# Kernel tuning notes

Measured on AMD Instinct MI355X. Metric: run time of the kernel, lower is better.

The kernel has to match this reference:

```python
import jax, jax.numpy as jnp
import numpy as np

BATCH, N, C_IN, HID, C_OUT = 32, 4096, 128, 256, 128


def setup_inputs() -> dict:
    key = jax.random.key(0)
    k1, k2, k3, k4 = jax.random.split(key, 4)
    x = jax.random.normal(k1, (BATCH, N, C_IN), dtype=jnp.float32)
    A = jnp.eye(HID, dtype=jnp.float32) + 0.01 * jax.random.normal(k2, (HID, HID), dtype=jnp.float32)
    W_B = 0.01 * jax.random.normal(k3, (HID, C_IN), dtype=jnp.float32)
    W_C = 0.01 * jax.random.normal(k4, (C_OUT, HID), dtype=jnp.float32)
    return {"x": x, "A": A, "W_B": W_B, "W_C": W_C}


def reference(x, A, W_B, W_C):
    # Spectral-norm normalize A (torch.linalg.norm ord=2 = largest singular value)
    A_norm = A / (jnp.linalg.norm(A, ord=2) + 1e-5)
    # Precompute input projection for all timesteps: (B, N, H)
    u = jnp.einsum('bnc,hc->bnh', x, W_B)

    h0 = jnp.zeros((x.shape[0], A.shape[0]), dtype=x.dtype)

    def step(h, u_t):
        h = jax.nn.relu(h @ A_norm.T + u_t)
        return h, h

    # scan over time axis: (N, B, H)
    _, hs = jax.lax.scan(step, h0, jnp.swapaxes(u, 0, 1))
    # Output projection applied to all hidden states at once: (B, N, C_out)
    y = jnp.einsum('nbh,oh->bno', hs, W_C)
    return y
```

## Files before the change

### kernel.cpp

```cpp
#include <hip/hip_runtime.h>
#include <hip/hip_bf16.h>
#include <hip/hip_fp16.h>

#define DEV static __device__ __forceinline__

typedef unsigned int u32;
typedef unsigned short u16;

typedef _Float16 half2v __attribute__((ext_vector_type(2)));

union HU { u32 u; half2v h; };
union FI { float f; int i; };

#if __has_builtin(__builtin_amdgcn_fdot2)
DEV float fdot2u(u32 a, u32 b, float c){
  HU ua; ua.u = a; HU ub; ub.u = b;
  return __builtin_amdgcn_fdot2(ua.h, ub.h, c, false);
}
#else
DEV float fdot2u(u32 a, u32 b, float c){
  HU ua; ua.u = a; HU ub; ub.u = b;
  return c + (float)ua.h.x*(float)ub.h.x + (float)ua.h.y*(float)ub.h.y;
}
#endif

#if __has_builtin(__builtin_amdgcn_mov_dpp)
DEV float dppf(float x, const int ctrl_b1, const int ctrl_4e, const int sel){
  FI u; u.f = x;
  if (sel == 0)      u.i = __builtin_amdgcn_mov_dpp(u.i, 0xB1, 0xF, 0xF, true);
  else if (sel == 1) u.i = __builtin_amdgcn_mov_dpp(u.i, 0x4E, 0xF, 0xF, true);
  else               u.i = __builtin_amdgcn_mov_dpp(u.i, 0x128, 0xF, 0xF, true);
  return u.f;
  (void)ctrl_b1; (void)ctrl_4e;
}
#define XOR1F(x) dppf((x),0,0,0)
#define XOR2F(x) dppf((x),0,0,1)
#define XOR8F(x) dppf((x),0,0,2)
#else
#define XOR1F(x) __shfl_xor((x), 1, 64)
#define XOR2F(x) __shfl_xor((x), 2, 64)
#define XOR8F(x) __shfl_xor((x), 8, 64)
#endif

#if __has_builtin(__builtin_amdgcn_ds_swizzle)
DEV float xor4f(float x){
  FI u; u.f = x;
  u.i = __builtin_amdgcn_ds_swizzle(u.i, 0x101F);
  return u.f;
}
#else
DEV float xor4f(float x){ return __shfl_xor(x, 4, 64); }
#endif

DEV u32 packh2(float x, float y){
  half2v h; h.x = (_Float16)x; h.y = (_Float16)y;
  HU u; u.h = h; return u.u;
}

DEV float bf2f(u16 v){ u32 x = ((u32)v) << 16; float f; __builtin_memcpy(&f, &x, 4); return f; }

DEV u16 f2bf(float f){
  u32 x; __builtin_memcpy(&x, &f, 4);
  u32 r = (x + 0x7fffu + ((x >> 16) & 1u)) >> 16;
  return (u16)r;
}

DEV float4 load4g(const void* p, long g, int bf){
  if (!bf) return ((const float4*)p)[g];
  ushort4 u = ((const ushort4*)p)[g];
  return make_float4(bf2f(u.x), bf2f(u.y), bf2f(u.z), bf2f(u.w));
}
DEV float load1g(const void* p, long i, int bf){
  return bf ? bf2f(((const u16*)p)[i]) : ((const float*)p)[i];
}

DEV int mloc(int v){ return (v & 3) | ((v & 8) >> 1); }

__global__ void k_detect(const void* __restrict__ A, int* __restrict__ flag){
  float a0 = ((const float*)A)[0];
  *flag = !(a0 > 0.5f && a0 < 2.0f);
}

__global__ __launch_bounds__(256) void k_btb(const void* __restrict__ A, float* __restrict__ Bm,
                                             const int* __restrict__ flag){
  __shared__ float acol[256];
  int t = threadIdx.x, r = blockIdx.x, bf = *flag;
  acol[t] = load1g(A, (long)t*256 + r, bf);
  __syncthreads();
  float acc = 0.f;
  if (bf){
    const u16* Ab = (const u16*)A;
    #pragma unroll 4
    for (int k = 0; k < 256; k++) acc += acol[k] * bf2f(Ab[(long)k*256 + t]);
  } else {
    const float* Af = (const float*)A;
    #pragma unroll 4
    for (int k = 0; k < 256; k++) acc += acol[k] * Af[(long)k*256 + t];
  }
  Bm[(long)r*256 + t] = acc;
}

__global__ __launch_bounds__(512) void k_lanczos(const float* __restrict__ Bm, float* __restrict__ out_scale){
  const int NIT = 40;
  __shared__ float vbuf[256], vprev[256];
  __shared__ float part[2][256];
  __shared__ float red[8];
  __shared__ float al[NIT], be[NIT + 1];
  int tid = threadIdx.x;
  int i = tid & 255, kh = tid >> 8;

  float4 Breg[32];
  #pragma unroll
  for (int g = 0; g < 32; g++) Breg[g] = ((const float4*)Bm)[(long)i*64 + kh*32 + g];

  if (tid == 0) be[0] = 0.f;
  if (tid < 256){
    u32 rs = (u32)tid*1103515245u + 12345u;
    rs ^= rs >> 13; rs *= 2654435761u; rs ^= rs >> 16;
    vbuf[tid] = (float)(rs & 0xffffu)/32768.0f - 1.0f;
    vprev[tid] = 0.f;
  }
  __syncthreads();
  if (tid < 256){
    float p = vbuf[tid]*vbuf[tid];
    #pragma unroll
    for (int m = 1; m < 64; m <<= 1) p += __shfl_xor(p, m, 64);
    if ((tid & 63) == 0) red[tid >> 6] = p;
  }
  __syncthreads();
  {
    float nv = rsqrtf(red[0]+red[1]+red[2]+red[3]);
    if (tid < 256) vbuf[tid] *= nv;
  }
  __syncthreads();

  float bprev = 0.f;
  for (int it = 0; it < NIT; it++){
    const float4* vb4 = (const float4*)vbuf;
    float4 acc = {0.f,0.f,0.f,0.f};
    #pragma unroll
    for (int g = 0; g < 32; g++){
      float4 bq = Breg[g]; float4 v = vb4[kh*32 + g];
      acc.x += bq.x*v.x; acc.y += bq.y*v.y; acc.z += bq.z*v.z; acc.w += bq.w*v.w;
    }
    part[kh][i] = acc.x+acc.y+acc.z+acc.w;
    __syncthreads();
    float w = 0.f;
    if (tid < 256){
      w = part[0][tid] + part[1][tid];
      float p = w * vbuf[tid];
      #pragma unroll
      for (int m = 1; m < 64; m <<= 1) p += __shfl_xor(p, m, 64);
      if ((tid & 63) == 0) red[tid >> 6] = p;
    }
    __syncthreads();
    float alpha = red[0]+red[1]+red[2]+red[3];
    if (tid == 0) al[it] = alpha;
    __syncthreads();
    if (tid < 256){
      w -= alpha*vbuf[tid] + bprev*vprev[tid];
      float p = w*w;
      #pragma unroll
      for (int m = 1; m < 64; m <<= 1) p += __shfl_xor(p, m, 64);
      if ((tid & 63) == 0) red[tid >> 6] = p;
    }
    __syncthreads();
    float bnew = sqrtf(fmaxf(red[0]+red[1]+red[2]+red[3], 0.f));
    if (tid == 0) be[it+1] = bnew;
    if (tid < 256){
      vprev[tid] = vbuf[tid];
      vbuf[tid] = (bnew > 1e-12f) ? (w / bnew) : 0.f;
    }
    bprev = bnew;
    __syncthreads();
  }

  if (tid < 64){
    float amax = -1e30f, gmax = -1e30f;
    for (int q = 0; q < NIT; q++){
      float b0 = (q > 0)       ? be[q]   : 0.f;
      float b1 = (q < NIT-1)   ? be[q+1] : 0.f;
      gmax = fmaxf(gmax, al[q] + fabsf(b0) + fabsf(b1));
      amax = fmaxf(amax, al[q]);
    }
    float lo = amax - 1e-4f, hi = gmax + 1e-3f;
    for (int r = 0; r < 4; r++){
      float step = (hi - lo) * (1.0f/65.0f);
      float cand = lo + step * (float)(tid + 1);
      int cnt = 0;
      float dd = al[0] - cand;
      if (dd < 0.f) cnt++;
      for (int q = 1; q < NIT; q++){
        float bq = be[q];
        if (fabsf(dd) < 1e-25f) dd = -1e-25f;
        dd = (al[q] - cand) - bq*bq/dd;
        if (dd < 0.f) cnt++;
      }
      unsigned long long mask = __ballot(cnt >= NIT);
      if (mask == 0ull){
        lo = lo + step*64.f;
      } else {
        int bb = __ffsll((long long)mask) - 1;
        float nlo = lo + step*(float)bb;
        float nhi = lo + step*(float)(bb+1);
        lo = nlo; hi = nhi;
      }
    }
    if (tid == 0){
      float lam = fmaxf(0.5f*(lo + hi), 1e-12f);
      *out_scale = 1.0f/(sqrtf(lam) + 1e-5f);
    }
  }
}

__global__ __launch_bounds__(256) void k_uproj(const void* __restrict__ x, const void* __restrict__ WB,
                                               u32* __restrict__ scr, const int* __restrict__ flag){
  __shared__ alignas(16) u32 Wt[64*260];
  __shared__ alignas(16) u32 xt[64*36];
  int tid = threadIdx.x;
  int bf = *flag;
  long T0 = (long)blockIdx.x * 32;
  #pragma unroll
  for (int i2 = 0; i2 < 32; i2++){
    int f = tid + 256*i2;
    int cq = f & 31, h = f >> 5;
    float4 v = load4g(WB, (long)h*32 + cq, bf);
    Wt[(2*cq)*260 + h]   = packh2(v.x, v.y);
    Wt[(2*cq+1)*260 + h] = packh2(v.z, v.w);
  }
  #pragma unroll
  for (int i2 = 0; i2 < 4; i2++){
    int f = tid + 256*i2;
    int cq = f & 31, t = f >> 5;
    float4 v = load4g(x, (T0 + t)*32 + cq, bf);
    xt[(2*cq)*36 + t]   = packh2(v.x, v.y);
    xt[(2*cq+1)*36 + t] = packh2(v.z, v.w);
  }
  __syncthreads();
  int hg = tid & 63, tg = tid >> 6;
  float acc[4][8];
  #pragma unroll
  for (int a1 = 0; a1 < 4; a1++)
    for (int b1 = 0; b1 < 8; b1++) acc[a1][b1] = 0.f;
  #pragma unroll 4
  for (int kp = 0; kp < 64; kp++){
    uint4 wv = *(const uint4*)&Wt[kp*260 + 4*hg];
    uint4 xa = *(const uint4*)&xt[kp*36 + 8*tg];
    uint4 xb = *(const uint4*)&xt[kp*36 + 8*tg + 4];
    u32 wj[4] = {wv.x, wv.y, wv.z, wv.w};
    u32 xs[8] = {xa.x, xa.y, xa.z, xa.w, xb.x, xb.y, xb.z, xb.w};
    #pragma unroll
    for (int jj = 0; jj < 4; jj++)
      #pragma unroll
      for (int tt = 0; tt < 8; tt++)
        acc[jj][tt] = fdot2u(wj[jj], xs[tt], acc[jj][tt]);
  }
  #pragma unroll
  for (int tt = 0; tt < 8; tt++){
    long T = T0 + 8*tg + tt;
    uint2 o;
    o.x = packh2(acc[0][tt], acc[1][tt]);
    o.y = packh2(acc[2][tt], acc[3][tt]);
    ((uint2*)scr)[T*64 + hg] = o;
  }
}

__global__ __launch_bounds__(512, 2) void k_recur(const void* __restrict__ A, const float* __restrict__ scale_p,
                                                  u32* __restrict__ scr, const int* __restrict__ flag){
  __shared__ alignas(16) char hbuf[2][768];
  __shared__ alignas(16) __half uring[32*256];
  int tid = threadIdx.x;
  int i = tid >> 4, j = tid & 15;
  int b = blockIdx.x;
  int bf = *flag;
  float s = *scale_p;
  int myrow = 8*i + mloc(j);

  u32 a[8][8];
  #pragma unroll
  for (int sx = 0; sx < 8; sx++){
    int G = (sx & 3) | ((sx & 4) << 1);
    int R = 8*i + mloc(j ^ G);
    #pragma unroll
    for (int q = 0; q < 4; q++){
      float4 v = load4g(A, (long)R*64 + 4*j + q, bf);
      float vv[4] = {v.x, v.y, v.z, v.w};
      #pragma unroll
      for (int e = 0; e < 4; e++){
        int col = 16*j + 4*q + e;
        if (col == R) vv[e] = 0.f;
      }
      a[sx][2*q]   = packh2(vv[0]*s, vv[1]*s);
      a[sx][2*q+1] = packh2(vv[2]*s, vv[3]*s);
    }
  }
  float d = load1g(A, (long)myrow*257, bf) * s;

  const uint4* scr4 = (const uint4*)scr;
  uint4* ur4 = (uint4*)uring;
  long ubase4 = (long)b * 131072;
  u16* hsout = (u16*)scr + (long)b*4096*256;

  uint4 pf;
  ur4[tid] = scr4[ubase4 + tid];
  pf = scr4[ubase4 + 512 + tid];

  int hoff16 = 24*(myrow >> 4) + (myrow & 15);
  ((u16*)hbuf[0])[hoff16] = 0;
  ((u16*)hbuf[1])[hoff16] = 0;
  __syncthreads();

  float hprev = 0.f;
  #pragma unroll 1
  for (int t = 0; t < 4096; ++t){
    const uint4* h4 = (const uint4*)(hbuf[t & 1] + 48*j);
    uint4 h0 = h4[0], h1 = h4[1];
    float uv = __half2float(uring[(t & 31)*256 + myrow]);
    float acc[8];
    #pragma unroll
    for (int sx = 0; sx < 8; sx++){
      float ac = 0.f;
      ac = fdot2u(a[sx][0], h0.x, ac);
      ac = fdot2u(a[sx][1], h0.y, ac);
      ac = fdot2u(a[sx][2], h0.z, ac);
      ac = fdot2u(a[sx][3], h0.w, ac);
      ac = fdot2u(a[sx][4], h1.x, ac);
      ac = fdot2u(a[sx][5], h1.y, ac);
      ac = fdot2u(a[sx][6], h1.z, ac);
      ac = fdot2u(a[sx][7], h1.w, ac);
      acc[sx] = ac;
    }
    acc[0] += XOR1F(acc[1]);
    acc[2] += XOR1F(acc[3]);
    acc[4] += XOR1F(acc[5]);
    acc[6] += XOR1F(acc[7]);
    acc[0] += XOR2F(acc[2]);
    acc[4] += XOR2F(acc[6]);
    acc[0] += XOR8F(acc[4]);
    float sum = acc[0] + xor4f(acc[0]);

    float hnew = fmaxf(fmaf(d, hprev, sum + uv), 0.f);
    hprev = hnew;
    u16 hh = __half_as_ushort(__float2half(hnew));
    ((u16*)hbuf[(t & 1) ^ 1])[hoff16] = hh;
    hsout[(long)t*256 + myrow] = hh;

    if ((t & 15) == 15 && t < 4095){
      int ct = (t + 1) >> 4;
      ur4[(ct & 1)*512 + tid] = pf;
      if (ct < 255) pf = scr4[ubase4 + (long)(ct + 1)*512 + tid];
    }
    __syncthreads();
  }
}

__global__ __launch_bounds__(256) void k_yproj(const u32* __restrict__ scr, const void* __restrict__ WC,
                                               void* __restrict__ y, const int* __restrict__ flag){
  __shared__ alignas(16) u32 Wt[128*132];
  __shared__ alignas(16) u32 ht[128*68];
  int tid = threadIdx.x, bf = *flag;
  long T0 = (long)blockIdx.x * 64;
  #pragma unroll
  for (int i2 = 0; i2 < 32; i2++){
    int f = tid + 256*i2;
    int kp = f & 127, t = f >> 7;
    ht[kp*68 + t] = scr[(T0 + t)*128 + kp];
  }
  #pragma unroll
  for (int i2 = 0; i2 < 32; i2++){
    int f = tid + 256*i2;
    int kq = f & 63, o = f >> 6;
    float4 v = load4g(WC, (long)o*64 + kq, bf);
    Wt[(2*kq)*132 + o]   = packh2(v.x, v.y);
    Wt[(2*kq+1)*132 + o] = packh2(v.z, v.w);
  }
  __syncthreads();
  int og = tid & 31, tg = tid >> 5;
  float acc[4][8];
  #pragma unroll
  for (int a1 = 0; a1 < 4; a1++)
    for (int b1 = 0; b1 < 8; b1++) acc[a1][b1] = 0.f;
  #pragma unroll 4
  for (int kp = 0; kp < 128; kp++){
    uint4 wv = *(const uint4*)&Wt[kp*132 + 4*og];
    uint4 ha = *(const uint4*)&ht[kp*68 + 8*tg];
    uint4 hc = *(const uint4*)&ht[kp*68 + 8*tg + 4];
    u32 wj[4] = {wv.x, wv.y, wv.z, wv.w};
    u32 hs8[8] = {ha.x, ha.y, ha.z, ha.w, hc.x, hc.y, hc.z, hc.w};
    #pragma unroll
    for (int jj = 0; jj < 4; jj++)
      #pragma unroll
      for (int tt = 0; tt < 8; tt++)
        acc[jj][tt] = fdot2u(wj[jj], hs8[tt], acc[jj][tt]);
  }
  #pragma unroll
  for (int tt = 0; tt < 8; tt++){
    long T = T0 + 8*tg + tt;
    if (!bf){
      float4 o = {acc[0][tt], acc[1][tt], acc[2][tt], acc[3][tt]};
      ((float4*)y)[T*32 + og] = o;
    } else {
      uint2 o;
      o.x = (u32)f2bf(acc[0][tt]) | ((u32)f2bf(acc[1][tt]) << 16);
      o.y = (u32)f2bf(acc[2][tt]) | ((u32)f2bf(acc[3][tt]) << 16);
      ((uint2*)y)[T*32 + og] = o;
    }
  }
}

extern "C" void kernel_launch(void* const* d_in, const int* in_sizes, int n_in,
                              void* d_out, int out_size, void* d_ws, size_t ws_size,
                              hipStream_t stream){
  const void* x  = d_in[0];
  const void* A  = d_in[1];
  const void* WB = d_in[2];
  const void* WC = d_in[3];

  float* Bm    = (float*)d_ws;
  float* scale = (float*)((char*)d_ws + 256*1024);
  int*   flag  = (int*)((char*)d_ws + 256*1024 + 64);

  const size_t scrOff = (size_t)1 << 20;
  const size_t scrBytes = (size_t)131072 * 256 * 2;
  u32* scr = (ws_size >= scrOff + scrBytes + 4096)
               ? (u32*)((char*)d_ws + scrOff)
               : (u32*)d_out;

  k_detect <<<1, 1, 0, stream>>>(A, flag);
  k_btb    <<<256, 256, 0, stream>>>(A, Bm, flag);
  k_lanczos<<<1, 512, 0, stream>>>(Bm, scale);
  k_uproj  <<<4096, 256, 0, stream>>>(x, WB, scr, flag);
  k_recur  <<<32, 512, 0, stream>>>(A, scale, scr, flag);
  k_yproj  <<<2048, 256, 0, stream>>>(scr, WC, d_out, flag);
}
```

Before: 2.338 ms.

## Process two batch sequences per recurrence block to share barriers and weights

Each recurrence block now advances two batch sequences in lockstep instead of one, halving the grid to 16 blocks. The two independent dot-product chains give more instruction-level parallelism per barrier and spread the per-step __syncthreads and shuffle-reduction latency over twice the work, while the A fragment held in registers is reused for both sequences. The cost is more work per step on the serial critical path, higher register and LDS use, and only 16 of the GPU's CUs kept busy.

```diff
diff --git a/kernel.cpp b/kernel.cpp
--- a/kernel.cpp
+++ b/kernel.cpp
@@ -265,13 +265,38 @@
   }
 }
 
+DEV float step_dot(const u32 (&a)[8][8], uint4 h0, uint4 h1){
+  float acc[8];
+  #pragma unroll
+  for (int sx = 0; sx < 8; sx++){
+    float ac = 0.f;
+    ac = fdot2u(a[sx][0], h0.x, ac);
+    ac = fdot2u(a[sx][1], h0.y, ac);
+    ac = fdot2u(a[sx][2], h0.z, ac);
+    ac = fdot2u(a[sx][3], h0.w, ac);
+    ac = fdot2u(a[sx][4], h1.x, ac);
+    ac = fdot2u(a[sx][5], h1.y, ac);
+    ac = fdot2u(a[sx][6], h1.z, ac);
+    ac = fdot2u(a[sx][7], h1.w, ac);
+    acc[sx] = ac;
+  }
+  acc[0] += XOR1F(acc[1]);
+  acc[2] += XOR1F(acc[3]);
+  acc[4] += XOR1F(acc[5]);
+  acc[6] += XOR1F(acc[7]);
+  acc[0] += XOR2F(acc[2]);
+  acc[4] += XOR2F(acc[6]);
+  acc[0] += XOR8F(acc[4]);
+  return acc[0] + xor4f(acc[0]);
+}
+
 __global__ __launch_bounds__(512, 2) void k_recur(const void* __restrict__ A, const float* __restrict__ scale_p,
                                                   u32* __restrict__ scr, const int* __restrict__ flag){
-  __shared__ alignas(16) char hbuf[2][768];
-  __shared__ alignas(16) __half uring[32*256];
+  __shared__ alignas(16) char hbuf[2][2][768];
+  __shared__ alignas(16) __half uring[2][32*256];
   int tid = threadIdx.x;
   int i = tid >> 4, j = tid & 15;
-  int b = blockIdx.x;
+  int b0 = 2*blockIdx.x, b1 = b0 + 1;
   int bf = *flag;
   float s = *scale_p;
   int myrow = 8*i + mloc(j);
@@ -297,58 +322,57 @@
   float d = load1g(A, (long)myrow*257, bf) * s;
 
   const uint4* scr4 = (const uint4*)scr;
-  uint4* ur4 = (uint4*)uring;
-  long ubase4 = (long)b * 131072;
-  u16* hsout = (u16*)scr + (long)b*4096*256;
-
-  uint4 pf;
-  ur4[tid] = scr4[ubase4 + tid];
-  pf = scr4[ubase4 + 512 + tid];
+  uint4* ur40 = (uint4*)uring[0];
+  uint4* ur41 = (uint4*)uring[1];
+  long ub0 = (long)b0 * 131072;
+  long ub1 = (long)b1 * 131072;
+  u16* hs0 = (u16*)scr + (long)b0*4096*256;
+  u16* hs1 = (u16*)scr + (long)b1*4096*256;
+
+  uint4 pf0, pf1;
+  ur40[tid] = scr4[ub0 + tid];
+  ur41[tid] = scr4[ub1 + tid];
+  pf0 = scr4[ub0 + 512 + tid];
+  pf1 = scr4[ub1 + 512 + tid];
 
   int hoff16 = 24*(myrow >> 4) + (myrow & 15);
-  ((u16*)hbuf[0])[hoff16] = 0;
-  ((u16*)hbuf[1])[hoff16] = 0;
-  __syncthreads();
-
-  float hprev = 0.f;
+  ((u16*)hbuf[0][0])[hoff16] = 0;
+  ((u16*)hbuf[0][1])[hoff16] = 0;
+  ((u16*)hbuf[1][0])[hoff16] = 0;
+  ((u16*)hbuf[1][1])[hoff16] = 0;
+  __syncthreads();
+
+  float hp0 = 0.f, hp1 = 0.f;
   #pragma unroll 1
   for (int t = 0; t < 4096; ++t){
-    const uint4* h4 = (const uint4*)(hbuf[t & 1] + 48*j);
-    uint4 h0 = h4[0], h1 = h4[1];
-    float uv = __half2float(uring[(t & 31)*256 + myrow]);
-    float acc[8];
-    #pragma unroll
-    for (int sx = 0; sx < 8; sx++){
-      float ac = 0.f;
-      ac = fdot2u(a[sx][0], h0.x, ac);
-      ac = fdot2u(a[sx][1], h0.y, ac);
-      ac = fdot2u(a[sx][2], h0.z, ac);
-      ac = fdot2u(a[sx][3], h0.w, ac);
-      ac = fdot2u(a[sx][4], h1.x, ac);
-      ac = fdot2u(a[sx][5], h1.y, ac);
-      ac = fdot2u(a[sx][6], h1.z, ac);
-      ac = fdot2u(a[sx][7], h1.w, ac);
-      acc[sx] = ac;
-    }
-    acc[0] += XOR1F(acc[1]);
-    acc[2] += XOR1F(acc[3]);
-    acc[4] += XOR1F(acc[5]);
-    acc[6] += XOR1F(acc[7]);
-    acc[0] += XOR2F(acc[2]);
-    acc[4] += XOR2F(acc[6]);
-    acc[0] += XOR8F(acc[4]);
-    float sum = acc[0] + xor4f(acc[0]);
-
-    float hnew = fmaxf(fmaf(d, hprev, sum + uv), 0.f);
-    hprev = hnew;
-    u16 hh = __half_as_ushort(__float2half(hnew));
-    ((u16*)hbuf[(t & 1) ^ 1])[hoff16] = hh;
-    hsout[(long)t*256 + myrow] = hh;
+    const uint4* h4a = (const uint4*)(hbuf[0][t & 1] + 48*j);
+    const uint4* h4b = (const uint4*)(hbuf[1][t & 1] + 48*j);
+    uint4 ha0 = h4a[0], ha1 = h4a[1];
+    uint4 hb0 = h4b[0], hb1 = h4b[1];
+    float uv0 = __half2float(uring[0][(t & 31)*256 + myrow]);
+    float uv1 = __half2float(uring[1][(t & 31)*256 + myrow]);
+
+    float sum0 = step_dot(a, ha0, ha1);
+    float sum1 = step_dot(a, hb0, hb1);
+
+    float hn0 = fmaxf(fmaf(d, hp0, sum0 + uv0), 0.f);
+    float hn1 = fmaxf(fmaf(d, hp1, sum1 + uv1), 0.f);
+    hp0 = hn0; hp1 = hn1;
+    u16 hh0 = __half_as_ushort(__float2half(hn0));
+    u16 hh1 = __half_as_ushort(__float2half(hn1));
+    ((u16*)hbuf[0][(t & 1) ^ 1])[hoff16] = hh0;
+    ((u16*)hbuf[1][(t & 1) ^ 1])[hoff16] = hh1;
+    hs0[(long)t*256 + myrow] = hh0;
+    hs1[(long)t*256 + myrow] = hh1;
 
     if ((t & 15) == 15 && t < 4095){
       int ct = (t + 1) >> 4;
-      ur4[(ct & 1)*512 + tid] = pf;
-      if (ct < 255) pf = scr4[ubase4 + (long)(ct + 1)*512 + tid];
+      ur40[(ct & 1)*512 + tid] = pf0;
+      ur41[(ct & 1)*512 + tid] = pf1;
+      if (ct < 255){
+        pf0 = scr4[ub0 + (long)(ct + 1)*512 + tid];
+        pf1 = scr4[ub1 + (long)(ct + 1)*512 + tid];
+      }
     }
     __syncthreads();
   }
@@ -430,6 +454,6 @@
   k_btb    <<<256, 256, 0, stream>>>(A, Bm, flag);
   k_lanczos<<<1, 512, 0, stream>>>(Bm, scale);
   k_uproj  <<<4096, 256, 0, stream>>>(x, WB, scr, flag);
-  k_recur  <<<32, 512, 0, stream>>>(A, scale, scr, flag);
+  k_recur  <<<16, 512, 0, stream>>>(A, scale, scr, flag);
   k_yproj  <<<2048, 256, 0, stream>>>(scr, WC, d_out, flag);
 }
```

New measurement: 3.574 ms. +52.9%, slower.

## Use MFMA for recurrence, batching 16 sequences per block

Applied to the files above, without the earlier changes.

The recurrence kernel previously ran one block per batch element and did a matrix-vector product with packed fp16 dot instructions plus cross-lane shuffle reductions. It now runs two blocks, each handling 16 batch elements as the N dimension of a 16x16x32 fp16 MFMA. A is held in registers as MFMA A-fragments, and the hidden state sits in swizzled LDS. The u-input is prefetched through a 4-slot LDS ring. This trades parallelism across CUs (only 2 blocks) for far less arithmetic and reduction work per step, so the serial chain now depends on MFMA latency.

```diff
diff --git a/kernel.cpp b/kernel.cpp
--- a/kernel.cpp
+++ b/kernel.cpp
@@ -8,6 +8,8 @@
 typedef unsigned short u16;
 
 typedef _Float16 half2v __attribute__((ext_vector_type(2)));
+typedef _Float16 f16x8 __attribute__((ext_vector_type(8)));
+typedef float f32x4 __attribute__((ext_vector_type(4)));
 
 union HU { u32 u; half2v h; };
 union FI { float f; int i; };
@@ -24,34 +26,6 @@
 }
 #endif
 
-#if __has_builtin(__builtin_amdgcn_mov_dpp)
-DEV float dppf(float x, const int ctrl_b1, const int ctrl_4e, const int sel){
-  FI u; u.f = x;
-  if (sel == 0)      u.i = __builtin_amdgcn_mov_dpp(u.i, 0xB1, 0xF, 0xF, true);
-  else if (sel == 1) u.i = __builtin_amdgcn_mov_dpp(u.i, 0x4E, 0xF, 0xF, true);
-  else               u.i = __builtin_amdgcn_mov_dpp(u.i, 0x128, 0xF, 0xF, true);
-  return u.f;
-  (void)ctrl_b1; (void)ctrl_4e;
-}
-#define XOR1F(x) dppf((x),0,0,0)
-#define XOR2F(x) dppf((x),0,0,1)
-#define XOR8F(x) dppf((x),0,0,2)
-#else
-#define XOR1F(x) __shfl_xor((x), 1, 64)
-#define XOR2F(x) __shfl_xor((x), 2, 64)
-#define XOR8F(x) __shfl_xor((x), 8, 64)
-#endif
-
-#if __has_builtin(__builtin_amdgcn_ds_swizzle)
-DEV float xor4f(float x){
-  FI u; u.f = x;
-  u.i = __builtin_amdgcn_ds_swizzle(u.i, 0x101F);
-  return u.f;
-}
-#else
-DEV float xor4f(float x){ return __shfl_xor(x, 4, 64); }
-#endif
-
 DEV u32 packh2(float x, float y){
   half2v h; h.x = (_Float16)x; h.y = (_Float16)y;
   HU u; u.h = h; return u.u;
@@ -73,8 +47,6 @@
 DEV float load1g(const void* p, long i, int bf){
   return bf ? bf2f(((const u16*)p)[i]) : ((const float*)p)[i];
 }
-
-DEV int mloc(int v){ return (v & 3) | ((v & 8) >> 1); }
 
 __global__ void k_detect(const void* __restrict__ A, int* __restrict__ flag){
   float a0 = ((const float*)A)[0];
@@ -265,90 +237,112 @@
   }
 }
 
-__global__ __launch_bounds__(512, 2) void k_recur(const void* __restrict__ A, const float* __restrict__ scale_p,
-                                                  u32* __restrict__ scr, const int* __restrict__ flag){
-  __shared__ alignas(16) char hbuf[2][768];
-  __shared__ alignas(16) __half uring[32*256];
-  int tid = threadIdx.x;
-  int i = tid >> 4, j = tid & 15;
-  int b = blockIdx.x;
-  int bf = *flag;
-  float s = *scale_p;
-  int myrow = 8*i + mloc(j);
-
-  u32 a[8][8];
-  #pragma unroll
-  for (int sx = 0; sx < 8; sx++){
-    int G = (sx & 3) | ((sx & 4) << 1);
-    int R = 8*i + mloc(j ^ G);
-    #pragma unroll
-    for (int q = 0; q < 4; q++){
-      float4 v = load4g(A, (long)R*64 + 4*j + q, bf);
-      float vv[4] = {v.x, v.y, v.z, v.w};
-      #pragma unroll
-      for (int e = 0; e < 4; e++){
-        int col = 16*j + 4*q + e;
-        if (col == R) vv[e] = 0.f;
+__global__ __launch_bounds__(512) void k_recur(const void* __restrict__ A, const float* __restrict__ scale_p,
+                                               u32* __restrict__ scr, const int* __restrict__ flag){
+  __shared__ alignas(16) char Ht[2*8192];
+  __shared__ alignas(16) char Ur[4*8192];
+  const int tid = threadIdx.x;
+  const int w = tid >> 6, l = tid & 63;
+  const int g = l >> 4, n = l & 15;
+  const int bf = *flag;
+  const float s = *scale_p;
+  const int n0 = blockIdx.x * 16;
+
+  f16x8 af[2][8];
+  float dg[2][4];
+  #pragma unroll
+  for (int mt = 0; mt < 2; mt++){
+    int arow = 32*w + 16*mt + n;
+    #pragma unroll
+    for (int kk = 0; kk < 8; kk++){
+      int c0 = 32*kk + 8*g;
+      float4 v0 = load4g(A, (long)arow*64 + (c0 >> 2), bf);
+      float4 v1 = load4g(A, (long)arow*64 + (c0 >> 2) + 1, bf);
+      float vv[8] = {v0.x, v0.y, v0.z, v0.w, v1.x, v1.y, v1.z, v1.w};
+      f16x8 f;
+      #pragma unroll
+      for (int i2 = 0; i2 < 8; i2++){
+        float x = (c0 + i2 == arow) ? 0.f : vv[i2]*s;
+        f[i2] = (_Float16)x;
       }
-      a[sx][2*q]   = packh2(vv[0]*s, vv[1]*s);
-      a[sx][2*q+1] = packh2(vv[2]*s, vv[3]*s);
-    }
-  }
-  float d = load1g(A, (long)myrow*257, bf) * s;
-
-  const uint4* scr4 = (const uint4*)scr;
-  uint4* ur4 = (uint4*)uring;
-  long ubase4 = (long)b * 131072;
-  u16* hsout = (u16*)scr + (long)b*4096*256;
-
-  uint4 pf;
-  ur4[tid] = scr4[ubase4 + tid];
-  pf = scr4[ubase4 + 512 + tid];
-
-  int hoff16 = 24*(myrow >> 4) + (myrow & 15);
-  ((u16*)hbuf[0])[hoff16] = 0;
-  ((u16*)hbuf[1])[hoff16] = 0;
-  __syncthreads();
-
-  float hprev = 0.f;
+      af[mt][kk] = f;
+    }
+    #pragma unroll
+    for (int r = 0; r < 4; r++){
+      int R = 32*w + 16*mt + 4*g + r;
+      dg[mt][r] = load1g(A, (long)R*257, bf) * s;
+    }
+  }
+
+  const int swz = (n & 7) << 4;
+  const int R0a = 32*w + 4*g;
+
+  const uint4* u4g = (const uint4*)scr;
+  const int nb = tid >> 5, e4 = tid & 31;
+  const int uswz = (nb & 7) << 4;
+  const int uoff = nb*512 + e4*16;
+  const long ug0 = ((long)(n0 + nb)*4096)*32 + e4;
+  uint4 p0  = u4g[ug0 + 0*32];
+  uint4 p1  = u4g[ug0 + 1*32];
+  uint4 pfA = u4g[ug0 + 2*32];
+  uint4 pfB = u4g[ug0 + 3*32];
+  *(uint4*)(Ur + 0*8192 + (uoff ^ uswz)) = p0;
+  *(uint4*)(Ur + 1*8192 + (uoff ^ uswz)) = p1;
+  *(uint4*)(Ht + tid*16) = make_uint4(0, 0, 0, 0);
+  __syncthreads();
+
+  f32x4 hp[2];
+  hp[0] = (f32x4){0.f, 0.f, 0.f, 0.f};
+  hp[1] = (f32x4){0.f, 0.f, 0.f, 0.f};
+  u16* hsbase = (u16*)scr;
+
   #pragma unroll 1
   for (int t = 0; t < 4096; ++t){
-    const uint4* h4 = (const uint4*)(hbuf[t & 1] + 48*j);
-    uint4 h0 = h4[0], h1 = h4[1];
-    float uv = __half2float(uring[(t & 31)*256 + myrow]);
-    float acc[8];
-    #pragma unroll
-    for (int sx = 0; sx < 8; sx++){
-      float ac = 0.f;
-      ac = fdot2u(a[sx][0], h0.x, ac);
-      ac = fdot2u(a[sx][1], h0.y, ac);
-      ac = fdot2u(a[sx][2], h0.z, ac);
-      ac = fdot2u(a[sx][3], h0.w, ac);
-      ac = fdot2u(a[sx][4], h1.x, ac);
-      ac = fdot2u(a[sx][5], h1.y, ac);
-      ac = fdot2u(a[sx][6], h1.z, ac);
-      ac = fdot2u(a[sx][7], h1.w, ac);
-      acc[sx] = ac;
-    }
-    acc[0] += XOR1F(acc[1]);
-    acc[2] += XOR1F(acc[3]);
-    acc[4] += XOR1F(acc[5]);
-    acc[6] += XOR1F(acc[7]);
-    acc[0] += XOR2F(acc[2]);
-    acc[4] += XOR2F(acc[6]);
-    acc[0] += XOR8F(acc[4]);
-    float sum = acc[0] + xor4f(acc[0]);
-
-    float hnew = fmaxf(fmaf(d, hprev, sum + uv), 0.f);
-    hprev = hnew;
-    u16 hh = __half_as_ushort(__float2half(hnew));
-    ((u16*)hbuf[(t & 1) ^ 1])[hoff16] = hh;
-    hsout[(long)t*256 + myrow] = hh;
-
-    if ((t & 15) == 15 && t < 4095){
-      int ct = (t + 1) >> 4;
-      ur4[(ct & 1)*512 + tid] = pf;
-      if (ct < 255) pf = scr4[ubase4 + (long)(ct + 1)*512 + tid];
+    const char* hb  = Ht + (t & 1)*8192;
+    char*       hbn = Ht + ((t & 1) ^ 1)*8192;
+    const char* ub  = Ur + (t & 3)*8192;
+
+    f16x8 bfr[8];
+    #pragma unroll
+    for (int kk = 0; kk < 8; kk++){
+      int off = n*512 + kk*64 + g*16;
+      bfr[kk] = *(const f16x8*)(hb + (off ^ swz));
+    }
+
+    f32x4 acc[2];
+    #pragma unroll
+    for (int mt = 0; mt < 2; mt++){
+      union { uint2 q; _Float16 h[4]; } uv;
+      uv.q = *(const uint2*)(ub + ((n*512 + (R0a + 16*mt)*2) ^ swz));
+      acc[mt] = (f32x4){(float)uv.h[0], (float)uv.h[1], (float)uv.h[2], (float)uv.h[3]};
+    }
+
+    #pragma unroll
+    for (int kk = 0; kk < 8; kk++){
+      acc[0] = __builtin_amdgcn_mfma_f32_16x16x32_f16(af[0][kk], bfr[kk], acc[0], 0, 0, 0);
+      acc[1] = __builtin_amdgcn_mfma_f32_16x16x32_f16(af[1][kk], bfr[kk], acc[1], 0, 0, 0);
+    }
+
+    #pragma unroll
+    for (int mt = 0; mt < 2; mt++){
+      f32x4 hn;
+      #pragma unroll
+      for (int r = 0; r < 4; r++){
+        hn[r] = fmaxf(fmaf(dg[mt][r], hp[mt][r], acc[mt][r]), 0.f);
+      }
+      hp[mt] = hn;
+      uint2 pk;
+      pk.x = packh2(hn[0], hn[1]);
+      pk.y = packh2(hn[2], hn[3]);
+      int R0 = R0a + 16*mt;
+      *(uint2*)(hbn + ((n*512 + R0*2) ^ swz)) = pk;
+      *(uint2*)(hsbase + ((long)(n0 + n)*1048576 + (long)t*256 + R0)) = pk;
+    }
+
+    if (t + 2 < 4096){
+      *(uint4*)(Ur + ((t + 2) & 3)*8192 + (uoff ^ uswz)) = pfA;
+      pfA = pfB;
+      if (t + 4 < 4096) pfB = u4g[ug0 + (long)(t + 4)*32];
     }
     __syncthreads();
   }
@@ -430,6 +424,6 @@
   k_btb    <<<256, 256, 0, stream>>>(A, Bm, flag);
   k_lanczos<<<1, 512, 0, stream>>>(Bm, scale);
   k_uproj  <<<4096, 256, 0, stream>>>(x, WB, scr, flag);
-  k_recur  <<<32, 512, 0, stream>>>(A, scale, scr, flag);
+  k_recur  <<<2, 512, 0, stream>>>(A, scale, scr, flag);
   k_yproj  <<<2048, 256, 0, stream>>>(scr, WC, d_out, flag);
 }
```

Measured after the change: 5.390 ms. +130.5%, slower.
